# Performance work log

Hardware: AMD Instinct MI355X
Metric: run time of the kernel (lower is better)

Reference implementation:

```python
import math
import jax, jax.numpy as jnp
import numpy as np

B, S, HID = 2, 1024, 1024
NH, HD = 16, 64
WIN = 4096
CACHE = 3072
EPS = 1e-5


def _clinear(xr, xi, Wr, Wi, br, bi):
    # complex linear: (xr + i xi)(Wr + i Wi)^T + (br + i bi)
    yr = xr @ Wr.T - xi @ Wi.T + br
    yi = xr @ Wi.T + xi @ Wr.T + bi
    return yr, yi


def _forward(hidden_re, hidden_im, K_cache_re, K_cache_im, V_cache_re, V_cache_im,
             gamma, beta_re, beta_im,
             q_Wr, q_Wi, q_br, q_bi, k_Wr, k_Wi, k_br, k_bi,
             v_Wr, v_Wi, v_br, v_bi, o_Wr, o_Wi, o_br, o_bi):
    batch, seq, _ = hidden_re.shape
    # --- complex LayerNorm: center complex mean, normalize by sqrt(E|x-mu|^2) ---
    mur = hidden_re.mean(-1, keepdims=True)
    mui = hidden_im.mean(-1, keepdims=True)
    cr = hidden_re - mur
    ci = hidden_im - mui
    inv = jax.lax.rsqrt((cr * cr + ci * ci).mean(-1, keepdims=True) + EPS)
    nr = cr * inv * gamma + beta_re
    ni = ci * inv * gamma + beta_im
    # --- projections ---
    Qr, Qi = _clinear(nr, ni, q_Wr, q_Wi, q_br, q_bi)
    Kr, Ki = _clinear(nr, ni, k_Wr, k_Wi, k_br, k_bi)
    Vr, Vi = _clinear(nr, ni, v_Wr, v_Wi, v_br, v_bi)
    Qr = Qr.reshape(batch, seq, NH, HD)
    Qi = Qi.reshape(batch, seq, NH, HD)
    Kr = Kr.reshape(batch, seq, NH, HD)
    Ki = Ki.reshape(batch, seq, NH, HD)
    Vr = Vr.reshape(batch, seq, NH, HD)
    Vi = Vi.reshape(batch, seq, NH, HD)
    # --- KV cache concat + window eviction (static shapes) ---
    cache_len = K_cache_re.shape[1]
    Kr = jnp.concatenate([K_cache_re, Kr], axis=1)
    Ki = jnp.concatenate([K_cache_im, Ki], axis=1)
    Vr = jnp.concatenate([V_cache_re, Vr], axis=1)
    Vi = jnp.concatenate([V_cache_im, Vi], axis=1)
    total_kv = Kr.shape[1]
    if total_kv > WIN:
        drop = total_kv - WIN
        Kr, Ki, Vr, Vi = Kr[:, drop:], Ki[:, drop:], Vr[:, drop:], Vi[:, drop:]
        cache_len = max(0, cache_len - drop)
        total_kv = WIN
    # --- Hermitian scores: Re(Q K^H) = Qr.Kr + Qi.Ki ---
    scale = 1.0 / math.sqrt(HD)
    scores = (jnp.einsum('bshd,bthd->bhst', Qr, Kr)
              + jnp.einsum('bshd,bthd->bhst', Qi, Ki)) * scale
    rows = jnp.arange(seq)[:, None]
    cols = jnp.arange(total_kv)[None, :]
    allowed = cols <= rows + cache_len  # causal within current chunk, full cache visible
    scores = jnp.where(allowed, scores, jnp.float32(-1e30))
    weights = jax.nn.softmax(scores, axis=-1)  # [B,NH,S,T]
    outr = jnp.einsum('bhst,bthd->bshd', weights, Vr).reshape(batch, seq, NH * HD)
    outi = jnp.einsum('bhst,bthd->bshd', weights, Vi).reshape(batch, seq, NH * HD)
    dr, di = _clinear(outr, outi, o_Wr, o_Wi, o_br, o_bi)
    out_re = hidden_re + dr
    out_im = hidden_im + di
    new_K_re, new_K_im = Kr[:, -WIN:], Ki[:, -WIN:]
    new_V_re, new_V_im = Vr[:, -WIN:], Vi[:, -WIN:]
    return out_re, out_im, new_K_re, new_K_im, new_V_re, new_V_im


def setup_inputs() -> dict:
    key = jax.random.key(0)
    ks = jax.random.split(key, 16)
    w = 0.02
    d = {
        'hidden_re': jax.random.normal(ks[0], (B, S, HID), jnp.float32),
        'hidden_im': jax.random.normal(ks[1], (B, S, HID), jnp.float32),
        'K_cache_re': jax.random.normal(ks[2], (B, CACHE, NH, HD), jnp.float32),
        'K_cache_im': jax.random.normal(ks[3], (B, CACHE, NH, HD), jnp.float32),
        'V_cache_re': jax.random.normal(ks[4], (B, CACHE, NH, HD), jnp.float32),
        'V_cache_im': jax.random.normal(ks[5], (B, CACHE, NH, HD), jnp.float32),
        'gamma': jnp.ones((HID,), jnp.float32),
        'beta_re': jnp.zeros((HID,), jnp.float32),
        'beta_im': jnp.zeros((HID,), jnp.float32),
    }
    for i, p in enumerate(['q', 'k', 'v', 'o']):
        d[p + '_Wr'] = jax.random.normal(ks[6 + 2 * i], (HID, HID), jnp.float32) * w
        d[p + '_Wi'] = jax.random.normal(ks[7 + 2 * i], (HID, HID), jnp.float32) * w
        d[p + '_br'] = jnp.zeros((HID,), jnp.float32)
        d[p + '_bi'] = jnp.zeros((HID,), jnp.float32)
    return d


def reference(hidden_re, hidden_im, K_cache_re, K_cache_im, V_cache_re, V_cache_im,
              gamma, beta_re, beta_im,
              q_Wr, q_Wi, q_br, q_bi, k_Wr, k_Wi, k_br, k_bi,
              v_Wr, v_Wi, v_br, v_bi, o_Wr, o_Wi, o_br, o_bi):
    return _forward(hidden_re, hidden_im, K_cache_re, K_cache_im, V_cache_re, V_cache_im,
                    gamma, beta_re, beta_im,
                    q_Wr, q_Wi, q_br, q_bi, k_Wr, k_Wi, k_br, k_bi,
                    v_Wr, v_Wi, v_br, v_bi, o_Wr, o_Wi, o_br, o_bi)
```

## Files before the change

kernel.cpp:

```cpp
#include <hip/hip_runtime.h>
#include <hip/hip_bf16.h>
#include <cstdint>
#include <cstddef>

typedef __bf16 bf16x8 __attribute__((ext_vector_type(8)));
typedef float  f32x4  __attribute__((ext_vector_type(4)));

__device__ __forceinline__ unsigned short f2bf(float f) {
  union { float f; unsigned u; } v; v.f = f;
  unsigned u = v.u;
  u += 0x7FFFu + ((u >> 16) & 1u);
  return (unsigned short)(u >> 16);
}

__device__ __forceinline__ unsigned short f2bf_cvt(float f) {
  __bf16 h = (__bf16)f;
  return __builtin_bit_cast(unsigned short, h);
}

struct alignas(16) US8 { unsigned short u[8]; };

__device__ __forceinline__ void g2lds16(const void* g, void* l) {
  __builtin_amdgcn_global_load_lds(
      (const __attribute__((address_space(1))) unsigned int*)g,
      (__attribute__((address_space(3))) unsigned int*)l, 16, 0, 0);
}

#define BB 2
#define SS 1024
#define HID 1024
#define NHH 16
#define HDD 64
#define TT 4096
#define CCH 3072
#define QSCALE (0.125f * 1.44269504088896f)

__global__ __launch_bounds__(256) void ln_kernel(
    const float* __restrict__ hre, const float* __restrict__ him,
    const float* __restrict__ gamma, const float* __restrict__ bre,
    const float* __restrict__ bim, unsigned short* __restrict__ Aln)
{
  int m = blockIdx.x;
  int tid = threadIdx.x;
  const float4 vr = ((const float4*)(hre + (size_t)m * HID))[tid];
  const float4 vi = ((const float4*)(him + (size_t)m * HID))[tid];
  float sr = vr.x + vr.y + vr.z + vr.w;
  float si = vi.x + vi.y + vi.z + vi.w;
  float sq = vr.x*vr.x + vr.y*vr.y + vr.z*vr.z + vr.w*vr.w
           + vi.x*vi.x + vi.y*vi.y + vi.z*vi.z + vi.w*vi.w;
  __shared__ float red[3][4];
  int lane = tid & 63, w = tid >> 6;
  for (int off = 32; off; off >>= 1) {
    sr += __shfl_down(sr, off, 64);
    si += __shfl_down(si, off, 64);
    sq += __shfl_down(sq, off, 64);
  }
  if (lane == 0) { red[0][w] = sr; red[1][w] = si; red[2][w] = sq; }
  __syncthreads();
  sr = red[0][0] + red[0][1] + red[0][2] + red[0][3];
  si = red[1][0] + red[1][1] + red[1][2] + red[1][3];
  sq = red[2][0] + red[2][1] + red[2][2] + red[2][3];
  float mur = sr * (1.f/1024.f), mui = si * (1.f/1024.f);
  float var = sq * (1.f/1024.f) - mur*mur - mui*mui;
  float inv = rsqrtf(var + 1e-5f);
  int k = tid * 4;
  float4 g  = ((const float4*)gamma)[tid];
  float4 br = ((const float4*)bre)[tid];
  float4 bi = ((const float4*)bim)[tid];
  ushort4 nr, ni;
  nr.x = f2bf((vr.x - mur) * inv * g.x + br.x);
  nr.y = f2bf((vr.y - mur) * inv * g.y + br.y);
  nr.z = f2bf((vr.z - mur) * inv * g.z + br.z);
  nr.w = f2bf((vr.w - mur) * inv * g.w + br.w);
  ni.x = f2bf((vi.x - mui) * inv * g.x + bi.x);
  ni.y = f2bf((vi.y - mui) * inv * g.y + bi.y);
  ni.z = f2bf((vi.z - mui) * inv * g.z + bi.z);
  ni.w = f2bf((vi.w - mui) * inv * g.w + bi.w);
  *(ushort4*)&Aln[(size_t)m * 2048 + k]        = nr;
  *(ushort4*)&Aln[(size_t)m * 2048 + 1024 + k] = ni;
}

__global__ __launch_bounds__(256) void wprep_kernel(
    const float* __restrict__ qWr, const float* __restrict__ qWi,
    const float* __restrict__ kWr, const float* __restrict__ kWi,
    const float* __restrict__ vWr, const float* __restrict__ vWi,
    const float* __restrict__ oWr, const float* __restrict__ oWi,
    unsigned short* __restrict__ Wc)
{
  int gid = blockIdx.x * 256 + threadIdx.x;
  int idx = gid * 8;
  int p   = idx >> 22;
  int rem = idx & 0x3FFFFF;
  int n   = rem >> 11;
  int k   = rem & 2047;
  const float* Wr; const float* Wi;
  switch (p) {
    case 0:  Wr = qWr; Wi = qWi; break;
    case 1:  Wr = kWr; Wi = kWi; break;
    case 2:  Wr = vWr; Wi = vWi; break;
    default: Wr = oWr; Wi = oWi; break;
  }
  const float* src; float sgn = 1.f;
  if (n < 1024) {
    if (k < 1024) src = Wr + (size_t)n * 1024 + k;
    else        { src = Wi + (size_t)n * 1024 + (k - 1024); sgn = -1.f; }
  } else {
    if (k < 1024) src = Wi + (size_t)(n - 1024) * 1024 + k;
    else          src = Wr + (size_t)(n - 1024) * 1024 + (k - 1024);
  }
  float4 a = ((const float4*)src)[0];
  float4 b = ((const float4*)src)[1];
  US8 o;
  o.u[0] = f2bf(a.x * sgn); o.u[1] = f2bf(a.y * sgn);
  o.u[2] = f2bf(a.z * sgn); o.u[3] = f2bf(a.w * sgn);
  o.u[4] = f2bf(b.x * sgn); o.u[5] = f2bf(b.y * sgn);
  o.u[6] = f2bf(b.z * sgn); o.u[7] = f2bf(b.w * sgn);
  *(US8*)&Wc[idx] = o;
}

__global__ __launch_bounds__(256) void bprep_kernel(
    const float* __restrict__ qbr, const float* __restrict__ qbi,
    const float* __restrict__ kbr, const float* __restrict__ kbi,
    const float* __restrict__ vbr, const float* __restrict__ vbi,
    const float* __restrict__ obr, const float* __restrict__ obi,
    float* __restrict__ bc)
{
  int idx = blockIdx.x * 256 + threadIdx.x;
  int p = idx >> 11, n = idx & 2047;
  const float* br; const float* bi;
  switch (p) {
    case 0:  br = qbr; bi = qbi; break;
    case 1:  br = kbr; bi = kbi; break;
    case 2:  br = vbr; bi = vbi; break;
    default: br = obr; bi = obi; break;
  }
  bc[idx] = (n < 1024) ? br[n] : bi[n - 1024];
}

__global__ __launch_bounds__(256) void gemm_qkv_kernel(
    const unsigned short* __restrict__ A, const unsigned short* __restrict__ Bm,
    const float* __restrict__ bias,
    unsigned short* __restrict__ Qp, unsigned short* __restrict__ Kp,
    float* __restrict__ out_Kre, float* __restrict__ out_Kim,
    float* __restrict__ out_Vre, float* __restrict__ out_Vim)
{
  __shared__ alignas(16) unsigned short As[128][32];
  __shared__ alignas(16) unsigned short Bs[128][32];
  const int K = 2048;
  int bm = blockIdx.y * 128;
  int bn = blockIdx.x * 128;
  int tid = threadIdx.x;
  int lane = tid & 63, w = tid >> 6;
  int wm = (w >> 1) * 64, wn = (w & 1) * 64;
  int l15 = lane & 15, q = lane >> 4;
  int lr = tid >> 2;
  int lc = (tid & 3) * 8;

  f32x4 acc[4][4] = {};

  for (int k0 = 0; k0 < K; k0 += 32) {
    g2lds16(&A [(size_t)(bm + lr)      * K + k0 + lc], (unsigned short*)As + 8*tid);
    g2lds16(&A [(size_t)(bm + lr + 64) * K + k0 + lc], (unsigned short*)As + 2048 + 8*tid);
    g2lds16(&Bm[(size_t)(bn + lr)      * K + k0 + lc], (unsigned short*)Bs + 8*tid);
    g2lds16(&Bm[(size_t)(bn + lr + 64) * K + k0 + lc], (unsigned short*)Bs + 2048 + 8*tid);
    __syncthreads();
    bf16x8 af[4], bfr[4];
#pragma unroll
    for (int i = 0; i < 4; i++) af[i]  = *(const bf16x8*)&As[wm + i*16 + l15][q*8];
#pragma unroll
    for (int i = 0; i < 4; i++) bfr[i] = *(const bf16x8*)&Bs[wn + i*16 + l15][q*8];
#pragma unroll
    for (int i = 0; i < 4; i++)
#pragma unroll
      for (int j = 0; j < 4; j++)
        acc[i][j] = __builtin_amdgcn_mfma_f32_16x16x32_bf16(af[i], bfr[j], acc[i][j], 0, 0, 0);
    __syncthreads();
  }

  const int sec = bn >> 11;
#pragma unroll
  for (int i = 0; i < 4; i++)
#pragma unroll
    for (int j = 0; j < 4; j++) {
      int n = bn + wn + j*16 + l15;
      float bv = bias[n];
      int col = n & 2047;
      int re = (col < 1024) ? 1 : 0;
      int h = (col & 1023) >> 6, d = col & 63;
      int d2 = re ? d : 64 + d;
#pragma unroll
      for (int r = 0; r < 4; r++) {
        int m = bm + wm + i*16 + q*4 + r;
        float val = acc[i][j][r] + bv;
        int b = m >> 10, s = m & 1023;
        int bh = b*16 + h;
        if (sec == 0) {
          Qp[((size_t)bh*1024 + s)*128 + d2] = f2bf(val * QSCALE);
        } else if (sec == 1) {
          int t = CCH + s;
          Kp[((size_t)bh*4096 + t)*128 + d2] = f2bf(val);
          float* dst = re ? out_Kre : out_Kim;
          dst[(((size_t)b*4096 + t)*16 + h)*64 + d] = val;
        } else {
          int t = CCH + s;
          float* dst = re ? out_Vre : out_Vim;
          dst[(((size_t)b*4096 + t)*16 + h)*64 + d] = val;
        }
      }
    }
}

__global__ __launch_bounds__(256) void gemm_oproj_kernel(
    const unsigned short* __restrict__ A, const unsigned short* __restrict__ Bm,
    const float* __restrict__ bias, const float* __restrict__ hre,
    const float* __restrict__ him, float* __restrict__ out)
{
  __shared__ alignas(16) unsigned short As[128][32];
  __shared__ alignas(16) unsigned short Bs[128][32];
  int bm = blockIdx.y * 128;
  int bn = blockIdx.x * 128;
  int tid = threadIdx.x;
  int lane = tid & 63, w = tid >> 6;
  int wm = (w >> 1) * 64, wn = (w & 1) * 64;
  int l15 = lane & 15, q = lane >> 4;
  int lr = tid >> 2;
  int lc = (tid & 3) * 8;
  const int K = 2048;

  f32x4 acc[4][4] = {};

  for (int k0 = 0; k0 < K; k0 += 32) {
    g2lds16(&A [(size_t)(bm + lr)      * K + k0 + lc], (unsigned short*)As + 8*tid);
    g2lds16(&A [(size_t)(bm + lr + 64) * K + k0 + lc], (unsigned short*)As + 2048 + 8*tid);
    g2lds16(&Bm[(size_t)(bn + lr)      * K + k0 + lc], (unsigned short*)Bs + 8*tid);
    g2lds16(&Bm[(size_t)(bn + lr + 64) * K + k0 + lc], (unsigned short*)Bs + 2048 + 8*tid);
    __syncthreads();
    bf16x8 af[4], bfr[4];
#pragma unroll
    for (int i = 0; i < 4; i++) af[i]  = *(const bf16x8*)&As[wm + i*16 + l15][q*8];
#pragma unroll
    for (int i = 0; i < 4; i++) bfr[i] = *(const bf16x8*)&Bs[wn + i*16 + l15][q*8];
#pragma unroll
    for (int i = 0; i < 4; i++)
#pragma unroll
      for (int j = 0; j < 4; j++)
        acc[i][j] = __builtin_amdgcn_mfma_f32_16x16x32_bf16(af[i], bfr[j], acc[i][j], 0, 0, 0);
    __syncthreads();
  }

#pragma unroll
  for (int i = 0; i < 4; i++)
#pragma unroll
    for (int j = 0; j < 4; j++) {
      int n = bn + wn + j*16 + l15;
      float bv = bias[n];
#pragma unroll
      for (int r = 0; r < 4; r++) {
        int m = bm + wm + i*16 + q*4 + r;
        float val = acc[i][j][r] + bv;
        if (n < 1024) out[(size_t)m * 1024 + n] = val + hre[(size_t)m * 1024 + n];
        else out[2097152 + (size_t)m * 1024 + (n - 1024)] = val + him[(size_t)m * 1024 + (n - 1024)];
      }
    }
}

__global__ __launch_bounds__(256) void pack_kcache_kernel(
    const float* __restrict__ c_re, const float* __restrict__ c_im,
    unsigned short* __restrict__ Kp,
    float* __restrict__ out_re, float* __restrict__ out_im)
{
  int bh = blockIdx.y;
  int idx = (blockIdx.x * 256 + threadIdx.x) * 4;
  int d2 = idx & 127;
  int t  = idx >> 7;
  int b = bh >> 4, h = bh & 15;
  int d = d2 & 63;
  bool im = d2 >= 64;
  const float* src = im ? c_im : c_re;
  float4 v = *(const float4*)&src[(((size_t)b * CCH + t) * 16 + h) * 64 + d];
  ushort4 o;
  o.x = f2bf(v.x); o.y = f2bf(v.y); o.z = f2bf(v.z); o.w = f2bf(v.w);
  *(ushort4*)&Kp[((size_t)bh * 4096 + t) * 128 + d2] = o;
  float* dst = im ? out_im : out_re;
  *(float4*)&dst[(((size_t)b * 4096 + t) * 16 + h) * 64 + d] = v;
}

__global__ __launch_bounds__(256) void pack_vt_fused_kernel(
    const float* __restrict__ Vc_re, const float* __restrict__ Vc_im,
    float* __restrict__ out_Vre, float* __restrict__ out_Vim,
    unsigned short* __restrict__ Vt)
{
  __shared__ float Ts[64][136];
  const int ty = blockIdx.x & 63;
  const int bh = blockIdx.x >> 6;
  const int b = bh >> 4, h = bh & 15;
  const int t0 = ty * 64;
  const int tid = threadIdx.x;
#pragma unroll
  for (int rr = 0; rr < 8; rr++) {
    int j = rr * 256 + tid;
    int t_loc = j >> 5, c = j & 31;
    int d2 = c * 4;
    int t = t0 + t_loc;
    int d = (d2 < 64) ? d2 : d2 - 64;
    float4 v;
    if (t < CCH) {
      const float* src = (d2 < 64) ? Vc_re : Vc_im;
      v = *(const float4*)&src[(((size_t)b * CCH + t) * 16 + h) * 64 + d];
      float* dst = (d2 < 64) ? out_Vre : out_Vim;
      *(float4*)&dst[(((size_t)b * 4096 + t) * 16 + h) * 64 + d] = v;
    } else {
      const float* src = (d2 < 64) ? out_Vre : out_Vim;
      v = *(const float4*)&src[(((size_t)b * 4096 + t) * 16 + h) * 64 + d];
    }
    *(float4*)&Ts[t_loc][d2] = v;
  }
  __syncthreads();
  const int d2 = tid >> 1, half = tid & 1;
  unsigned short tmp[32];
#pragma unroll
  for (int i = 0; i < 32; i++) tmp[i] = f2bf(Ts[half*32 + i][d2]);
  size_t dst = (size_t)bh * 128 * 4096 + (size_t)d2 * 4096 + t0 + half*32;
#pragma unroll
  for (int kq = 0; kq < 4; kq++)
    *(US8*)&Vt[dst + kq*8] = *(US8*)&tmp[kq*8];
}

__global__ __launch_bounds__(256) void attn_kernel(
    const unsigned short* __restrict__ Qp, const unsigned short* __restrict__ Kp,
    const unsigned short* __restrict__ Vt, float* __restrict__ Opart,
    float* __restrict__ Lpart)
{
  const int bh   = blockIdx.x;
  const int sblk = blockIdx.y;
  const int tpar = blockIdx.z;
  const int s0 = sblk * 128;
  const int tid = threadIdx.x;
  const int lane = tid & 63, w = tid >> 6;
  const int l15 = lane & 15, q = lane >> 4;

  __shared__ alignas(16) unsigned short Ks[2][64][128];
  __shared__ alignas(16) unsigned short Vs[2][128][64];
  __shared__ alignas(16) unsigned short Ps[4][32][64];

  bf16x8 qf[2][4];
#pragma unroll
  for (int mi = 0; mi < 2; mi++) {
    const size_t qb = ((size_t)bh * 1024 + s0 + w*32 + mi*16 + l15) * 128;
#pragma unroll
    for (int kc = 0; kc < 4; kc++)
      qf[mi][kc] = *(const bf16x8*)&Qp[qb + kc*32 + q*8];
  }

  f32x4 oacc[2][8] = {};
  float lsum[2][4] = {};

  const size_t kpb = (size_t)bh * 4096 * 128;
  const size_t vtb = (size_t)bh * 128 * 4096;
  const int n_tiles = 2*sblk + 50;
  const int n_safe  = n_tiles - 2;

  auto issue = [&](int buf, int t0) {
#pragma unroll
    for (int kk = 0; kk < 4; kk++) {
      int j = (w*4 + kk)*64 + lane;
      int r = j >> 4, p = j & 15, c = p ^ (r & 7);
      g2lds16(&Kp[kpb + (size_t)(t0 + r) * 128 + c*8],
              (unsigned short*)&Ks[buf][0][0] + (size_t)j * 8);
    }
#pragma unroll
    for (int kk = 0; kk < 4; kk++) {
      int j = (w*4 + kk)*64 + lane;
      int r = j >> 3, p = j & 7, c = p ^ (r & 7);
      g2lds16(&Vt[vtb + (size_t)r * 4096 + t0 + c*8],
              (unsigned short*)&Vs[buf][0][0] + (size_t)j * 8);
    }
  };

  int buf = 0;
  issue(0, tpar * 64);

  for (int it = tpar; it < n_tiles; it += 2) {
    __syncthreads();
    if (it + 2 < n_tiles) issue(buf ^ 1, (it + 2) * 64);

    f32x4 sacc[2][4] = {};
    __builtin_amdgcn_s_setprio(1);
#pragma unroll
    for (int kc = 0; kc < 4; kc++) {
      bf16x8 kf[4];
#pragma unroll
      for (int nc = 0; nc < 4; nc++)
        kf[nc] = *(const bf16x8*)&Ks[buf][nc*16 + l15][((kc*4 + q) ^ (l15 & 7)) * 8];
#pragma unroll
      for (int mi = 0; mi < 2; mi++)
#pragma unroll
        for (int nc = 0; nc < 4; nc++)
          sacc[mi][nc] = __builtin_amdgcn_mfma_f32_16x16x32_bf16(qf[mi][kc], kf[nc], sacc[mi][nc], 0, 0, 0);
    }
    __builtin_amdgcn_s_setprio(0);

    const bool safe = (it < n_safe);
    const int t0 = it << 6;
#pragma unroll
    for (int mi = 0; mi < 2; mi++)
#pragma unroll
      for (int r = 0; r < 4; r++) {
        const int rr = mi*16 + q*4 + r;
        const int rel = s0 + w*32 + rr + CCH - t0;
        float ls = 0.f;
#pragma unroll
        for (int nc = 0; nc < 4; nc++) {
          float p;
          asm("v_exp_f32 %0, %1" : "=v"(p) : "v"(sacc[mi][nc][r]));
          if (!safe && (nc*16 + l15 > rel)) p = 0.f;
          ls += p;
          int cch = (nc*2 + (l15 >> 3)) ^ ((q << 1) | (r & 1));
          Ps[w][rr][cch*8 + (l15 & 7)] = f2bf_cvt(p);
        }
        lsum[mi][r] += ls;
      }

#pragma unroll
    for (int kch = 0; kch < 2; kch++) {
      bf16x8 pf[2];
#pragma unroll
      for (int mi = 0; mi < 2; mi++) {
        int rr = mi*16 + l15;
        int sw = (((l15 >> 2) & 3) << 1) | (l15 & 1);
        pf[mi] = *(const bf16x8*)&Ps[w][rr][((kch*4 + q) ^ sw) * 8];
      }
      __builtin_amdgcn_s_setprio(1);
#pragma unroll
      for (int dc = 0; dc < 8; dc++) {
        int d2 = dc*16 + l15;
        bf16x8 vfr = *(const bf16x8*)&Vs[buf][d2][((kch*4 + q) ^ (l15 & 7)) * 8];
#pragma unroll
        for (int mi = 0; mi < 2; mi++)
          oacc[mi][dc] = __builtin_amdgcn_mfma_f32_16x16x32_bf16(pf[mi], vfr, oacc[mi][dc], 0, 0, 0);
      }
      __builtin_amdgcn_s_setprio(0);
    }
    buf ^= 1;
  }

  const size_t pb = ((size_t)tpar * 32 + bh) * 1024 + s0 + w*32;
#pragma unroll
  for (int mi = 0; mi < 2; mi++)
#pragma unroll
    for (int r = 0; r < 4; r++) {
      float l = lsum[mi][r];
      l += __shfl_xor(l, 1, 64);
      l += __shfl_xor(l, 2, 64);
      l += __shfl_xor(l, 4, 64);
      l += __shfl_xor(l, 8, 64);
      if (l15 == 0) Lpart[pb + mi*16 + q*4 + r] = l;
    }
#pragma unroll
  for (int mi = 0; mi < 2; mi++)
#pragma unroll
    for (int dc = 0; dc < 8; dc++)
#pragma unroll
      for (int r = 0; r < 4; r++)
        Opart[(pb + mi*16 + q*4 + r) * 128 + dc*16 + l15] = oacc[mi][dc][r];
}

__global__ __launch_bounds__(256) void attn_combine_kernel(
    const float* __restrict__ Opart, const float* __restrict__ Lpart,
    unsigned short* __restrict__ Ao)
{
  const size_t TS = 4194304ull;
  int gid = blockIdx.x * 256 + threadIdx.x;
  int idx = gid * 8;
  int m = idx >> 11, n0 = idx & 2047;
  int b = m >> 10, s = m & 1023;
  int h, d2_0;
  if (n0 < 1024) { h = n0 >> 6; d2_0 = n0 & 63; }
  else { h = (n0 - 1024) >> 6; d2_0 = 64 + ((n0 - 1024) & 63); }
  int bh = b*16 + h;
  size_t ob = ((size_t)bh * 1024 + s) * 128 + d2_0;
  float l0 = Lpart[(size_t)bh * 1024 + s];
  float l1 = Lpart[32768 + (size_t)bh * 1024 + s];
  float inv = 1.f / (l0 + l1);
  float4 x0 = *(const float4*)&Opart[ob];
  float4 x1 = *(const float4*)&Opart[ob + 4];
  float4 y0 = *(const float4*)&Opart[ob + TS];
  float4 y1 = *(const float4*)&Opart[ob + TS + 4];
  US8 o;
  o.u[0] = f2bf((x0.x + y0.x) * inv); o.u[1] = f2bf((x0.y + y0.y) * inv);
  o.u[2] = f2bf((x0.z + y0.z) * inv); o.u[3] = f2bf((x0.w + y0.w) * inv);
  o.u[4] = f2bf((x1.x + y1.x) * inv); o.u[5] = f2bf((x1.y + y1.y) * inv);
  o.u[6] = f2bf((x1.z + y1.z) * inv); o.u[7] = f2bf((x1.w + y1.w) * inv);
  *(US8*)&Ao[idx] = o;
}

extern "C" void kernel_launch(void* const* d_in, const int* in_sizes, int n_in,
                              void* d_out, int out_size, void* d_ws, size_t ws_size,
                              hipStream_t stream)
{
  (void)in_sizes; (void)n_in; (void)out_size; (void)ws_size;
  const float* hre = (const float*)d_in[0];
  const float* him = (const float*)d_in[1];
  const float* Kcr = (const float*)d_in[2];
  const float* Kci = (const float*)d_in[3];
  const float* Vcr = (const float*)d_in[4];
  const float* Vci = (const float*)d_in[5];
  const float* gamma = (const float*)d_in[6];
  const float* bre = (const float*)d_in[7];
  const float* bim = (const float*)d_in[8];
  const float* qWr = (const float*)d_in[9];
  const float* qWi = (const float*)d_in[10];
  const float* qbr = (const float*)d_in[11];
  const float* qbi = (const float*)d_in[12];
  const float* kWr = (const float*)d_in[13];
  const float* kWi = (const float*)d_in[14];
  const float* kbr = (const float*)d_in[15];
  const float* kbi = (const float*)d_in[16];
  const float* vWr = (const float*)d_in[17];
  const float* vWi = (const float*)d_in[18];
  const float* vbr = (const float*)d_in[19];
  const float* vbi = (const float*)d_in[20];
  const float* oWr = (const float*)d_in[21];
  const float* oWi = (const float*)d_in[22];
  const float* obr = (const float*)d_in[23];
  const float* obi = (const float*)d_in[24];
  float* out = (float*)d_out;

  char* ws = (char*)d_ws;
  size_t off = 0;
  auto carve = [&](size_t bytes) {
    char* p = ws + off;
    off += (bytes + 255) & ~(size_t)255;
    return p;
  };
  unsigned short* Aln  = (unsigned short*)carve(2048ull * 2048 * 2);
  unsigned short* Wc   = (unsigned short*)carve(4ull * 2048 * 2048 * 2);
  float*          bc   = (float*)carve(4ull * 2048 * 4);
  unsigned short* Qp   = (unsigned short*)carve(4194304ull * 2);
  unsigned short* Kp   = (unsigned short*)carve(16777216ull * 2);
  unsigned short* Vt   = (unsigned short*)carve(16777216ull * 2);
  unsigned short* Ao   = (unsigned short*)carve(2048ull * 2048 * 2);
  float*          Opart= (float*)carve(2ull * 32 * 1024 * 128 * 4);
  float*          Lpart= (float*)carve(2ull * 32 * 1024 * 4);

  float* out_Kre = out + 4194304;
  float* out_Kim = out + 4194304 + 8388608;
  float* out_Vre = out + 4194304 + 2 * 8388608;
  float* out_Vim = out + 4194304 + 3 * 8388608;

  hipLaunchKernelGGL(ln_kernel, dim3(2048), dim3(256), 0, stream,
                     hre, him, gamma, bre, bim, Aln);
  hipLaunchKernelGGL(wprep_kernel, dim3(8192), dim3(256), 0, stream,
                     qWr, qWi, kWr, kWi, vWr, vWi, oWr, oWi, Wc);
  hipLaunchKernelGGL(bprep_kernel, dim3(32), dim3(256), 0, stream,
                     qbr, qbi, kbr, kbi, vbr, vbi, obr, obi, bc);
  hipLaunchKernelGGL(gemm_qkv_kernel, dim3(48, 16), dim3(256), 0, stream,
                     Aln, Wc, bc, Qp, Kp, out_Kre, out_Kim, out_Vre, out_Vim);
  hipLaunchKernelGGL(pack_kcache_kernel, dim3(384, 32), dim3(256), 0, stream,
                     Kcr, Kci, Kp, out_Kre, out_Kim);
  hipLaunchKernelGGL(pack_vt_fused_kernel, dim3(2048), dim3(256), 0, stream,
                     Vcr, Vci, out_Vre, out_Vim, Vt);
  hipLaunchKernelGGL(attn_kernel, dim3(32, 8, 2), dim3(256), 0, stream,
                     Qp, Kp, Vt, Opart, Lpart);
  hipLaunchKernelGGL(attn_combine_kernel, dim3(2048), dim3(256), 0, stream,
                     Opart, Lpart, Ao);
  hipLaunchKernelGGL(gemm_oproj_kernel, dim3(16, 16), dim3(256), 0, stream,
                     Ao, Wc + 3ull * 2048 * 2048, bc + 3 * 2048, hre, him, out);
}
```

Baseline: 601.6 us.

## Split attention KV loop three ways with 32-wide tiles

The attention kernel now uses 32-key tiles instead of 64 and splits the KV range across three grid-z partitions instead of two. The combine kernel sums three partial outputs and denominators. The intent is more workgroups for better CU occupancy and smaller LDS per block, which may allow more resident blocks. The cost is more loop iterations, a shorter MFMA chain per barrier, extra partial-result traffic, and reuse of the Aln buffer for Ao. The per-partition tile count must also stay consistent with the masking logic.

```diff
diff --git a/kernel.cpp b/kernel.cpp
--- a/kernel.cpp
+++ b/kernel.cpp
@@ -339,9 +339,9 @@
   const int lane = tid & 63, w = tid >> 6;
   const int l15 = lane & 15, q = lane >> 4;
 
-  __shared__ alignas(16) unsigned short Ks[2][64][128];
-  __shared__ alignas(16) unsigned short Vs[2][128][64];
-  __shared__ alignas(16) unsigned short Ps[4][32][64];
+  __shared__ alignas(16) unsigned short Ks[2][32][128];
+  __shared__ alignas(16) unsigned short Vs[2][128][32];
+  __shared__ alignas(16) unsigned short Ps[4][32][40];
 
   bf16x8 qf[2][4];
 #pragma unroll
@@ -357,51 +357,51 @@
 
   const size_t kpb = (size_t)bh * 4096 * 128;
   const size_t vtb = (size_t)bh * 128 * 4096;
-  const int n_tiles = 2*sblk + 50;
-  const int n_safe  = n_tiles - 2;
+  const int n_tiles = 4*sblk + 100;
+  const int n_safe  = n_tiles - 4;
 
   auto issue = [&](int buf, int t0) {
 #pragma unroll
-    for (int kk = 0; kk < 4; kk++) {
-      int j = (w*4 + kk)*64 + lane;
+    for (int kk = 0; kk < 2; kk++) {
+      int j = (w*2 + kk)*64 + lane;
       int r = j >> 4, p = j & 15, c = p ^ (r & 7);
       g2lds16(&Kp[kpb + (size_t)(t0 + r) * 128 + c*8],
               (unsigned short*)&Ks[buf][0][0] + (size_t)j * 8);
     }
 #pragma unroll
-    for (int kk = 0; kk < 4; kk++) {
-      int j = (w*4 + kk)*64 + lane;
-      int r = j >> 3, p = j & 7, c = p ^ (r & 7);
+    for (int kk = 0; kk < 2; kk++) {
+      int j = (w*2 + kk)*64 + lane;
+      int r = j >> 2, p = j & 3, c = p ^ (r & 3);
       g2lds16(&Vt[vtb + (size_t)r * 4096 + t0 + c*8],
               (unsigned short*)&Vs[buf][0][0] + (size_t)j * 8);
     }
   };
 
   int buf = 0;
-  issue(0, tpar * 64);
-
-  for (int it = tpar; it < n_tiles; it += 2) {
+  issue(0, tpar * 32);
+
+  for (int it = tpar; it < n_tiles; it += 3) {
     __syncthreads();
-    if (it + 2 < n_tiles) issue(buf ^ 1, (it + 2) * 64);
-
-    f32x4 sacc[2][4] = {};
+    if (it + 3 < n_tiles) issue(buf ^ 1, (it + 3) * 32);
+
+    f32x4 sacc[2][2] = {};
     __builtin_amdgcn_s_setprio(1);
 #pragma unroll
     for (int kc = 0; kc < 4; kc++) {
-      bf16x8 kf[4];
-#pragma unroll
-      for (int nc = 0; nc < 4; nc++)
+      bf16x8 kf[2];
+#pragma unroll
+      for (int nc = 0; nc < 2; nc++)
         kf[nc] = *(const bf16x8*)&Ks[buf][nc*16 + l15][((kc*4 + q) ^ (l15 & 7)) * 8];
 #pragma unroll
       for (int mi = 0; mi < 2; mi++)
 #pragma unroll
-        for (int nc = 0; nc < 4; nc++)
+        for (int nc = 0; nc < 2; nc++)
           sacc[mi][nc] = __builtin_amdgcn_mfma_f32_16x16x32_bf16(qf[mi][kc], kf[nc], sacc[mi][nc], 0, 0, 0);
     }
     __builtin_amdgcn_s_setprio(0);
 
     const bool safe = (it < n_safe);
-    const int t0 = it << 6;
+    const int t0 = it << 5;
 #pragma unroll
     for (int mi = 0; mi < 2; mi++)
 #pragma unroll
@@ -410,37 +410,30 @@
         const int rel = s0 + w*32 + rr + CCH - t0;
         float ls = 0.f;
 #pragma unroll
-        for (int nc = 0; nc < 4; nc++) {
+        for (int nc = 0; nc < 2; nc++) {
           float p;
           asm("v_exp_f32 %0, %1" : "=v"(p) : "v"(sacc[mi][nc][r]));
           if (!safe && (nc*16 + l15 > rel)) p = 0.f;
           ls += p;
-          int cch = (nc*2 + (l15 >> 3)) ^ ((q << 1) | (r & 1));
-          Ps[w][rr][cch*8 + (l15 & 7)] = f2bf_cvt(p);
+          Ps[w][rr][nc*16 + l15] = f2bf_cvt(p);
         }
         lsum[mi][r] += ls;
       }
 
-#pragma unroll
-    for (int kch = 0; kch < 2; kch++) {
-      bf16x8 pf[2];
-#pragma unroll
-      for (int mi = 0; mi < 2; mi++) {
-        int rr = mi*16 + l15;
-        int sw = (((l15 >> 2) & 3) << 1) | (l15 & 1);
-        pf[mi] = *(const bf16x8*)&Ps[w][rr][((kch*4 + q) ^ sw) * 8];
-      }
-      __builtin_amdgcn_s_setprio(1);
-#pragma unroll
-      for (int dc = 0; dc < 8; dc++) {
-        int d2 = dc*16 + l15;
-        bf16x8 vfr = *(const bf16x8*)&Vs[buf][d2][((kch*4 + q) ^ (l15 & 7)) * 8];
-#pragma unroll
-        for (int mi = 0; mi < 2; mi++)
-          oacc[mi][dc] = __builtin_amdgcn_mfma_f32_16x16x32_bf16(pf[mi], vfr, oacc[mi][dc], 0, 0, 0);
-      }
-      __builtin_amdgcn_s_setprio(0);
-    }
+    bf16x8 pf[2];
+#pragma unroll
+    for (int mi = 0; mi < 2; mi++)
+      pf[mi] = *(const bf16x8*)&Ps[w][mi*16 + l15][q*8];
+    __builtin_amdgcn_s_setprio(1);
+#pragma unroll
+    for (int dc = 0; dc < 8; dc++) {
+      int d2 = dc*16 + l15;
+      bf16x8 vfr = *(const bf16x8*)&Vs[buf][d2][(q ^ (d2 & 3)) * 8];
+#pragma unroll
+      for (int mi = 0; mi < 2; mi++)
+        oacc[mi][dc] = __builtin_amdgcn_mfma_f32_16x16x32_bf16(pf[mi], vfr, oacc[mi][dc], 0, 0, 0);
+    }
+    __builtin_amdgcn_s_setprio(0);
     buf ^= 1;
   }
 
@@ -481,16 +474,19 @@
   size_t ob = ((size_t)bh * 1024 + s) * 128 + d2_0;
   float l0 = Lpart[(size_t)bh * 1024 + s];
   float l1 = Lpart[32768 + (size_t)bh * 1024 + s];
-  float inv = 1.f / (l0 + l1);
+  float l2 = Lpart[65536 + (size_t)bh * 1024 + s];
+  float inv = 1.f / (l0 + l1 + l2);
   float4 x0 = *(const float4*)&Opart[ob];
   float4 x1 = *(const float4*)&Opart[ob + 4];
   float4 y0 = *(const float4*)&Opart[ob + TS];
   float4 y1 = *(const float4*)&Opart[ob + TS + 4];
+  float4 z0 = *(const float4*)&Opart[ob + 2*TS];
+  float4 z1 = *(const float4*)&Opart[ob + 2*TS + 4];
   US8 o;
-  o.u[0] = f2bf((x0.x + y0.x) * inv); o.u[1] = f2bf((x0.y + y0.y) * inv);
-  o.u[2] = f2bf((x0.z + y0.z) * inv); o.u[3] = f2bf((x0.w + y0.w) * inv);
-  o.u[4] = f2bf((x1.x + y1.x) * inv); o.u[5] = f2bf((x1.y + y1.y) * inv);
-  o.u[6] = f2bf((x1.z + y1.z) * inv); o.u[7] = f2bf((x1.w + y1.w) * inv);
+  o.u[0] = f2bf((x0.x + y0.x + z0.x) * inv); o.u[1] = f2bf((x0.y + y0.y + z0.y) * inv);
+  o.u[2] = f2bf((x0.z + y0.z + z0.z) * inv); o.u[3] = f2bf((x0.w + y0.w + z0.w) * inv);
+  o.u[4] = f2bf((x1.x + y1.x + z1.x) * inv); o.u[5] = f2bf((x1.y + y1.y + z1.y) * inv);
+  o.u[6] = f2bf((x1.z + y1.z + z1.z) * inv); o.u[7] = f2bf((x1.w + y1.w + z1.w) * inv);
   *(US8*)&Ao[idx] = o;
 }
 
@@ -539,9 +535,10 @@
   unsigned short* Qp   = (unsigned short*)carve(4194304ull * 2);
   unsigned short* Kp   = (unsigned short*)carve(16777216ull * 2);
   unsigned short* Vt   = (unsigned short*)carve(16777216ull * 2);
-  unsigned short* Ao   = (unsigned short*)carve(2048ull * 2048 * 2);
-  float*          Opart= (float*)carve(2ull * 32 * 1024 * 128 * 4);
-  float*          Lpart= (float*)carve(2ull * 32 * 1024 * 4);
+  float*          Opart= (float*)carve(3ull * 32 * 1024 * 128 * 4);
+  float*          Lpart= (float*)carve(3ull * 32 * 1024 * 4);
+
+  unsigned short* Ao = Aln;
 
   float* out_Kre = out + 4194304;
   float* out_Kim = out + 4194304 + 8388608;
@@ -560,7 +557,7 @@
                      Kcr, Kci, Kp, out_Kre, out_Kim);
   hipLaunchKernelGGL(pack_vt_fused_kernel, dim3(2048), dim3(256), 0, stream,
                      Vcr, Vci, out_Vre, out_Vim, Vt);
-  hipLaunchKernelGGL(attn_kernel, dim3(32, 8, 2), dim3(256), 0, stream,
+  hipLaunchKernelGGL(attn_kernel, dim3(32, 8, 3), dim3(256), 0, stream,
                      Qp, Kp, Vt, Opart, Lpart);
   hipLaunchKernelGGL(attn_combine_kernel, dim3(2048), dim3(256), 0, stream,
                      Opart, Lpart, Ao);
```

Result: no change. 598.6 us (-0.5%).
